# Optimization experiments

Hardware: AMD Instinct MI355X
Metric: run time of the kernel (lower is better)

Reference implementation:

```python
import jax, jax.numpy as jnp
import numpy as np

G, M_PER_GROUP, K, N = 8, 2048, 4096, 4096  # experts, tokens/expert, d_model, expert out dim


def setup_inputs() -> dict:
    key = jax.random.key(0)
    k1, k2, k3, k4 = jax.random.split(key, 4)
    T = G * M_PER_GROUP
    # int8 quantized activations [total_tokens, K] and per-expert weights [G, N, K] ('NT' layout)
    i8_left_tensor = jax.random.randint(k1, (T, K), -127, 128, dtype=jnp.int32).astype(jnp.int8)
    i8_right_tensors = jax.random.randint(k2, (G, N, K), -127, 128, dtype=jnp.int32).astype(jnp.int8)
    # per-token and per-(group, out-channel) dequant scales
    left_scales = jax.random.uniform(k3, (T,), jnp.float32, 0.001, 0.02)
    right_scales = jax.random.uniform(k4, (G, N), jnp.float32, 0.001, 0.02)
    tokens_per_group = jnp.full((G,), M_PER_GROUP, dtype=jnp.int32)
    return {
        "i8_left_tensor": i8_left_tensor,
        "i8_right_tensors": i8_right_tensors,
        "left_scales": left_scales,
        "right_scales": right_scales,
        "tokens_per_group": tokens_per_group,
    }


def reference(i8_left_tensor, i8_right_tensors, left_scales, right_scales, tokens_per_group):
    # moe_w8a8_group_gemm, 'NT': per group g, out_g = (A_g @ B_g^T) * ls_g[:, None] * rs_g[None, :] -> fp16
    g, n, k = i8_right_tensors.shape
    t = i8_left_tensor.shape[0]
    m = t // g  # equal-sized groups (tokens_per_group is constant M_PER_GROUP)
    a = i8_left_tensor.reshape(g, m, k).astype(jnp.float32)   # [G, M, K]
    b = i8_right_tensors.astype(jnp.float32)                  # [G, N, K]
    acc = jnp.einsum('gmk,gnk->gmn', a, b)                    # int8xint8 accum in f32
    ls = left_scales.reshape(g, m, 1)
    rs = right_scales[:, None, :]
    out = (acc * ls * rs).astype(jnp.float16)                 # fused dequant epilogue
    return out.reshape(t, n)
```

## Files before the change

kernel.cpp:

```cpp
#include <hip/hip_runtime.h>

#define GG 8
#define MPG 2048
#define KD 4096
#define ND 4096

using i32x4 = __attribute__((ext_vector_type(4))) int;

__device__ __forceinline__ int pack4(i32x4 v) {
  return (int)((unsigned)(v[0] & 0xff) | ((unsigned)(v[1] & 0xff) << 8) |
               ((unsigned)(v[2] & 0xff) << 16) | ((unsigned)(v[3] & 0xff) << 24));
}

__global__ void conv_kernel(const int* __restrict__ src, char* __restrict__ dst, long nelem) {
  long t = (long)blockIdx.x * blockDim.x + threadIdx.x;
  long stride = (long)gridDim.x * blockDim.x;
  for (long e = t * 16; e < nelem; e += stride * 16) {
    i32x4 x0 = *(const i32x4*)(src + e);
    i32x4 x1 = *(const i32x4*)(src + e + 4);
    i32x4 x2 = *(const i32x4*)(src + e + 8);
    i32x4 x3 = *(const i32x4*)(src + e + 12);
    i32x4 p;
    p[0] = pack4(x0); p[1] = pack4(x1); p[2] = pack4(x2); p[3] = pack4(x3);
    *(i32x4*)(dst + e) = p;
  }
}

__device__ __forceinline__ void gload_lds16(const void* g, void* l) {
  __builtin_amdgcn_global_load_lds(
      (const __attribute__((address_space(1))) unsigned int*)g,
      (__attribute__((address_space(3))) unsigned int*)l, 16, 0, 0);
}

constexpr int NT = KD / 128;

__global__ __launch_bounds__(512, 2) void gemm256_i8(
    const char* __restrict__ Aall,
    const char* __restrict__ Ball,
    const float* __restrict__ ls,
    const float* __restrict__ rs,
    float* __restrict__ out,
    int g0, int nwg)
{
  extern __shared__ char lds[];

  const int tid  = threadIdx.x;
  const int lane = tid & 63;
  const int wave = tid >> 6;

  int bid = blockIdx.x;
  int wg  = (bid & 7) * (nwg >> 3) + (bid >> 3);
  const int gl = wg >> 7;
  const int rr_ = wg & 127;
  const int bm = (rr_ >> 4) * 256;
  const int bn = (rr_ & 15) * 256;
  const int g  = g0 + gl;

  const int srow = tid >> 3;
  const int scol = ((tid & 7) << 4) ^ ((srow & 7) << 4);
  const char* Ag = Aall + ((size_t)gl * MPG + bm) * KD;
  const char* Bg = Ball + ((size_t)gl * ND  + bn) * KD;
  const char* pa[4]; const char* pb[4];
#pragma unroll
  for (int i = 0; i < 4; ++i) {
    pa[i] = Ag + (size_t)(i * 64 + srow) * KD + scol;
    pb[i] = Bg + (size_t)(i * 64 + srow) * KD + scol;
  }
  char* wbase = lds + wave * 1024;

  auto stage = [&](int buf, int kt) {
    const int ko = kt << 7;
    char* d = wbase + buf * 65536;
#pragma unroll
    for (int i = 0; i < 4; ++i) gload_lds16(pa[i] + ko, d + i * 8192);
#pragma unroll
    for (int i = 0; i < 4; ++i) gload_lds16(pb[i] + ko, d + 32768 + i * 8192);
  };

  const int wm = wave >> 2;
  const int wn = wave & 3;
  const int r16 = lane & 15;
  const int klane = (lane >> 4) << 4;
  const int sx = (r16 & 7) << 4;
  const char* aBase0 = lds + (size_t)(wm * 128 + r16) * 128;
  const char* bBase0 = lds + 32768 + (size_t)(wn * 64 + r16) * 128;

  i32x4 acc[8][4] = {};

  auto compute = [&](int buf) {
    const char* pA = aBase0 + buf * 65536;
    const char* pB = bBase0 + buf * 65536;
#pragma unroll
    for (int ks = 0; ks < 2; ++ks) {
      const int kx = ((ks << 6) + klane) ^ sx;
      i32x4 bf[4], af[8];
#pragma unroll
      for (int n = 0; n < 4; ++n) bf[n] = *(const i32x4*)(pB + n * 2048 + kx);
#pragma unroll
      for (int m = 0; m < 8; ++m) af[m] = *(const i32x4*)(pA + m * 2048 + kx);
      __builtin_amdgcn_s_setprio(1);
#pragma unroll
      for (int m = 0; m < 8; ++m)
#pragma unroll
        for (int n = 0; n < 4; ++n)
          acc[m][n] = __builtin_amdgcn_mfma_i32_16x16x64_i8(af[m], bf[n], acc[m][n], 0, 0, 0);
      __builtin_amdgcn_s_setprio(0);
    }
  };

  stage(0, 0);
  stage(1, 1);
#pragma unroll 1
  for (int kt = 0; kt < NT; ++kt) {
    const int cur = kt & 1;
    if (kt + 1 < NT) { asm volatile("s_waitcnt vmcnt(8)" ::: "memory"); }
    else             { asm volatile("s_waitcnt vmcnt(0)" ::: "memory"); }
    __builtin_amdgcn_s_barrier();
    asm volatile("" ::: "memory");
    compute(cur);
    asm volatile("" ::: "memory");
    __builtin_amdgcn_s_barrier();
    asm volatile("" ::: "memory");
    if (kt + 2 < NT) stage(cur, kt + 2);
  }

  const size_t orow0 = (size_t)g * MPG + bm + wm * 128 + ((lane >> 4) << 2);
  const int col0 = bn + wn * 64 + r16;
  float rsv[4];
#pragma unroll
  for (int n = 0; n < 4; ++n) rsv[n] = rs[(size_t)g * ND + col0 + n * 16];
#pragma unroll
  for (int m = 0; m < 8; ++m) {
#pragma unroll
    for (int q = 0; q < 4; ++q) {
      size_t row = orow0 + m * 16 + q;
      float lsv = ls[row];
#pragma unroll
      for (int n = 0; n < 4; ++n)
        out[row * ND + col0 + n * 16] = (float)acc[m][n][q] * lsv * rsv[n];
    }
  }
}

constexpr int BM = 128, BN = 128, BK = 64;

template<bool DIRECT>
__global__ __launch_bounds__(256) void gemm_i8(
    const void* __restrict__ Aptr, const void* __restrict__ Bptr,
    const float* __restrict__ ls, const float* __restrict__ rs,
    float* __restrict__ out, int g0)
{
  __shared__ char lA[BM * BK];
  __shared__ char lB[BN * BK];

  const int gl = blockIdx.z;
  const int g = g0 + gl;
  const int bm = blockIdx.y * BM;
  const int bn = blockIdx.x * BN;
  const int tid = threadIdx.x;
  const int lane = tid & 63;
  const int wave = tid >> 6;
  const int wr = (wave >> 1) * 64;
  const int wc = (wave & 1) * 64;
  const int r16 = lane & 15;
  const int kb = (lane >> 4) * 16;

  i32x4 acc[4][4] = {};

  if constexpr (!DIRECT) {
    const char* Ag = (const char*)Aptr + ((size_t)gl * MPG + bm) * KD;
    const char* Bg = (const char*)Bptr + ((size_t)gl * ND + bn) * KD;
    const int srow = tid >> 2;
    const int skoff = (tid & 3) * 16;
    const char* pa0 = Ag + (size_t)srow * KD + skoff;
    const char* pa1 = Ag + (size_t)(srow + 64) * KD + skoff;
    const char* pb0 = Bg + (size_t)srow * KD + skoff;
    const char* pb1 = Bg + (size_t)(srow + 64) * KD + skoff;
    char* la0 = lA + wave * 1024;
    char* la1 = lA + 4096 + wave * 1024;
    char* lb0 = lB + wave * 1024;
    char* lb1 = lB + 4096 + wave * 1024;

    for (int k0 = 0; k0 < KD; k0 += BK) {
      gload_lds16(pa0 + k0, la0);
      gload_lds16(pa1 + k0, la1);
      gload_lds16(pb0 + k0, lb0);
      gload_lds16(pb1 + k0, lb1);
      __syncthreads();
      i32x4 af[4], bf[4];
#pragma unroll
      for (int m = 0; m < 4; ++m) af[m] = *(const i32x4*)(lA + (wr + m * 16 + r16) * BK + kb);
#pragma unroll
      for (int n = 0; n < 4; ++n) bf[n] = *(const i32x4*)(lB + (wc + n * 16 + r16) * BK + kb);
#pragma unroll
      for (int m = 0; m < 4; ++m)
#pragma unroll
        for (int n = 0; n < 4; ++n)
          acc[m][n] = __builtin_amdgcn_mfma_i32_16x16x64_i8(af[m], bf[n], acc[m][n], 0, 0, 0);
      __syncthreads();
    }
  } else {
    const int* Ag = (const int*)Aptr + ((size_t)gl * MPG + bm) * KD;
    const int* Bg = (const int*)Bptr + ((size_t)gl * ND + bn) * KD;
    const int drow = tid >> 1;
    const int dk = (tid & 1) * 32;

    for (int k0 = 0; k0 < KD; k0 += BK) {
      int pa[8], pb[8];
#pragma unroll
      for (int j = 0; j < 8; ++j) pa[j] = pack4(*(const i32x4*)(Ag + (size_t)drow * KD + k0 + dk + j * 4));
#pragma unroll
      for (int j = 0; j < 8; ++j) pb[j] = pack4(*(const i32x4*)(Bg + (size_t)drow * KD + k0 + dk + j * 4));
      __syncthreads();
      *(i32x4*)(lA + drow * 64 + dk)      = *(i32x4*)(pa);
      *(i32x4*)(lA + drow * 64 + dk + 16) = *(i32x4*)(pa + 4);
      *(i32x4*)(lB + drow * 64 + dk)      = *(i32x4*)(pb);
      *(i32x4*)(lB + drow * 64 + dk + 16) = *(i32x4*)(pb + 4);
      __syncthreads();
      i32x4 af[4], bf[4];
#pragma unroll
      for (int m = 0; m < 4; ++m) af[m] = *(const i32x4*)(lA + (wr + m * 16 + r16) * BK + kb);
#pragma unroll
      for (int n = 0; n < 4; ++n) bf[n] = *(const i32x4*)(lB + (wc + n * 16 + r16) * BK + kb);
#pragma unroll
      for (int m = 0; m < 4; ++m)
#pragma unroll
        for (int n = 0; n < 4; ++n)
          acc[m][n] = __builtin_amdgcn_mfma_i32_16x16x64_i8(af[m], bf[n], acc[m][n], 0, 0, 0);
    }
  }

  const size_t trow0 = (size_t)g * MPG + bm + wr + (lane >> 4) * 4;
  const int col0 = bn + wc + r16;
  float rsv[4];
#pragma unroll
  for (int n = 0; n < 4; ++n) rsv[n] = rs[(size_t)g * ND + col0 + n * 16];
#pragma unroll
  for (int m = 0; m < 4; ++m) {
#pragma unroll
    for (int q = 0; q < 4; ++q) {
      size_t row = trow0 + m * 16 + q;
      float lsv = ls[row];
#pragma unroll
      for (int n = 0; n < 4; ++n)
        out[row * ND + col0 + n * 16] = (float)acc[m][n][q] * lsv * rsv[n];
    }
  }
}

extern "C" void kernel_launch(void* const* d_in, const int* in_sizes, int n_in,
                              void* d_out, int out_size, void* d_ws, size_t ws_size,
                              hipStream_t stream) {
  const int* A32 = (const int*)d_in[0];
  const int* B32 = (const int*)d_in[1];
  const float* ls = (const float*)d_in[2];
  const float* rs = (const float*)d_in[3];
  float* out = (float*)d_out;

  const size_t aE = (size_t)GG * MPG * KD;
  const size_t bE = (size_t)GG * ND * KD;
  const size_t aSlab = (size_t)MPG * KD;
  const size_t bSlab = (size_t)ND * KD;

  const int smem = 131072;
  static_assert(131072 == 2 * (32768 + 32768), "lds layout");
  bool big_lds_ok =
      hipFuncSetAttribute((const void*)gemm256_i8,
                          hipFuncAttributeMaxDynamicSharedMemorySize, smem) == hipSuccess;

  if (d_ws && ws_size >= aE + bE) {
    char* wsA = (char*)d_ws;
    char* wsB = wsA + aE;
    conv_kernel<<<8192, 256, 0, stream>>>(A32, wsA, (long)aE);
    conv_kernel<<<16384, 256, 0, stream>>>(B32, wsB, (long)bE);
    if (big_lds_ok) {
      gemm256_i8<<<1024, 512, smem, stream>>>(wsA, wsB, ls, rs, out, 0, 1024);
    } else {
      dim3 grid(ND / BN, MPG / BM, GG);
      gemm_i8<false><<<grid, dim3(256), 0, stream>>>(wsA, wsB, ls, rs, out, 0);
    }
  } else if (d_ws && ws_size >= aSlab + bSlab) {
    char* wsA = (char*)d_ws;
    char* wsB = wsA + aSlab;
    for (int gidx = 0; gidx < GG; ++gidx) {
      conv_kernel<<<2048, 256, 0, stream>>>(A32 + (size_t)gidx * aSlab, wsA, (long)aSlab);
      conv_kernel<<<4096, 256, 0, stream>>>(B32 + (size_t)gidx * bSlab, wsB, (long)bSlab);
      if (big_lds_ok) {
        gemm256_i8<<<128, 512, smem, stream>>>(wsA, wsB, ls, rs, out, gidx, 128);
      } else {
        dim3 grid(ND / BN, MPG / BM, 1);
        gemm_i8<false><<<grid, dim3(256), 0, stream>>>(wsA, wsB, ls, rs, out, gidx);
      }
    }
  } else {
    dim3 grid(ND / BN, MPG / BM, GG);
    gemm_i8<true><<<grid, dim3(256), 0, stream>>>(A32, B32, ls, rs, out, 0);
  }
}
```

Baseline: 499.5 us.

## Split k-tile into four barrier-separated phases with interleaved next-tile prefetch

Restructures the GEMM main loop from a two-stage-ahead double buffer into a one-stage-ahead schedule where each 128-wide k-tile is processed in four phases of 16 MFMAs. The A and B global-to-LDS loads for the next tile are issued in separate phases between LDS fragment reads and MFMA bursts. The intent is to interleave memory issue with compute and reduce register pressure for fragments. The cost is more barriers per iteration and a shallower prefetch, which may expose global load latency.

```diff
diff --git a/kernel.cpp b/kernel.cpp
--- a/kernel.cpp
+++ b/kernel.cpp
@@ -32,6 +32,8 @@
       (__attribute__((address_space(3))) unsigned int*)l, 16, 0, 0);
 }
 
+#define CFENCE() asm volatile("" ::: "memory")
+
 constexpr int NT = KD / 128;
 
 __global__ __launch_bounds__(512, 2) void gemm256_i8(
@@ -68,13 +70,17 @@
   }
   char* wbase = lds + wave * 1024;
 
-  auto stage = [&](int buf, int kt) {
+  auto stageA = [&](int buf, int kt) {
     const int ko = kt << 7;
     char* d = wbase + buf * 65536;
 #pragma unroll
     for (int i = 0; i < 4; ++i) gload_lds16(pa[i] + ko, d + i * 8192);
-#pragma unroll
-    for (int i = 0; i < 4; ++i) gload_lds16(pb[i] + ko, d + 32768 + i * 8192);
+  };
+  auto stageB = [&](int buf, int kt) {
+    const int ko = kt << 7;
+    char* d = wbase + buf * 65536 + 32768;
+#pragma unroll
+    for (int i = 0; i < 4; ++i) gload_lds16(pb[i] + ko, d + i * 8192);
   };
 
   const int wm = wave >> 2;
@@ -87,41 +93,75 @@
 
   i32x4 acc[8][4] = {};
 
-  auto compute = [&](int buf) {
-    const char* pA = aBase0 + buf * 65536;
-    const char* pB = bBase0 + buf * 65536;
-#pragma unroll
-    for (int ks = 0; ks < 2; ++ks) {
-      const int kx = ((ks << 6) + klane) ^ sx;
-      i32x4 bf[4], af[8];
-#pragma unroll
-      for (int n = 0; n < 4; ++n) bf[n] = *(const i32x4*)(pB + n * 2048 + kx);
-#pragma unroll
-      for (int m = 0; m < 8; ++m) af[m] = *(const i32x4*)(pA + m * 2048 + kx);
-      __builtin_amdgcn_s_setprio(1);
-#pragma unroll
-      for (int m = 0; m < 8; ++m)
-#pragma unroll
-        for (int n = 0; n < 4; ++n)
-          acc[m][n] = __builtin_amdgcn_mfma_i32_16x16x64_i8(af[m], bf[n], acc[m][n], 0, 0, 0);
-      __builtin_amdgcn_s_setprio(0);
-    }
-  };
-
-  stage(0, 0);
-  stage(1, 1);
+  stageA(0, 0); stageB(0, 0);
+  asm volatile("s_waitcnt vmcnt(0)" ::: "memory");
+  __builtin_amdgcn_s_barrier();
+  CFENCE();
+
 #pragma unroll 1
   for (int kt = 0; kt < NT; ++kt) {
-    const int cur = kt & 1;
-    if (kt + 1 < NT) { asm volatile("s_waitcnt vmcnt(8)" ::: "memory"); }
-    else             { asm volatile("s_waitcnt vmcnt(0)" ::: "memory"); }
-    __builtin_amdgcn_s_barrier();
-    asm volatile("" ::: "memory");
-    compute(cur);
-    asm volatile("" ::: "memory");
-    __builtin_amdgcn_s_barrier();
-    asm volatile("" ::: "memory");
-    if (kt + 2 < NT) stage(cur, kt + 2);
+    const int c = kt & 1;
+    const char* pA = aBase0 + c * 65536;
+    const char* pB = bBase0 + c * 65536;
+    const int kx0 = klane ^ sx;
+    const int kx1 = (64 + klane) ^ sx;
+    const bool pre = (kt + 1 < NT);
+    i32x4 af[4], bf[4];
+
+#pragma unroll
+    for (int n = 0; n < 4; ++n) bf[n] = *(const i32x4*)(pB + n * 2048 + kx0);
+#pragma unroll
+    for (int m = 0; m < 4; ++m) af[m] = *(const i32x4*)(pA + m * 2048 + kx0);
+    if (pre) stageA(c ^ 1, kt + 1);
+    CFENCE(); __builtin_amdgcn_s_barrier(); CFENCE();
+    __builtin_amdgcn_s_setprio(1);
+#pragma unroll
+    for (int m = 0; m < 4; ++m)
+#pragma unroll
+      for (int n = 0; n < 4; ++n)
+        acc[m][n] = __builtin_amdgcn_mfma_i32_16x16x64_i8(af[m], bf[n], acc[m][n], 0, 0, 0);
+    __builtin_amdgcn_s_setprio(0);
+    CFENCE(); __builtin_amdgcn_s_barrier(); CFENCE();
+
+#pragma unroll
+    for (int m = 0; m < 4; ++m) af[m] = *(const i32x4*)(pA + (4 + m) * 2048 + kx0);
+    if (pre) stageB(c ^ 1, kt + 1);
+    CFENCE(); __builtin_amdgcn_s_barrier(); CFENCE();
+    __builtin_amdgcn_s_setprio(1);
+#pragma unroll
+    for (int m = 0; m < 4; ++m)
+#pragma unroll
+      for (int n = 0; n < 4; ++n)
+        acc[4 + m][n] = __builtin_amdgcn_mfma_i32_16x16x64_i8(af[m], bf[n], acc[4 + m][n], 0, 0, 0);
+    __builtin_amdgcn_s_setprio(0);
+    CFENCE(); __builtin_amdgcn_s_barrier(); CFENCE();
+
+#pragma unroll
+    for (int n = 0; n < 4; ++n) bf[n] = *(const i32x4*)(pB + n * 2048 + kx1);
+#pragma unroll
+    for (int m = 0; m < 4; ++m) af[m] = *(const i32x4*)(pA + m * 2048 + kx1);
+    CFENCE(); __builtin_amdgcn_s_barrier(); CFENCE();
+    __builtin_amdgcn_s_setprio(1);
+#pragma unroll
+    for (int m = 0; m < 4; ++m)
+#pragma unroll
+      for (int n = 0; n < 4; ++n)
+        acc[m][n] = __builtin_amdgcn_mfma_i32_16x16x64_i8(af[m], bf[n], acc[m][n], 0, 0, 0);
+    __builtin_amdgcn_s_setprio(0);
+    CFENCE(); __builtin_amdgcn_s_barrier(); CFENCE();
+
+#pragma unroll
+    for (int m = 0; m < 4; ++m) af[m] = *(const i32x4*)(pA + (4 + m) * 2048 + kx1);
+    asm volatile("s_waitcnt vmcnt(0)" ::: "memory");
+    CFENCE(); __builtin_amdgcn_s_barrier(); CFENCE();
+    __builtin_amdgcn_s_setprio(1);
+#pragma unroll
+    for (int m = 0; m < 4; ++m)
+#pragma unroll
+      for (int n = 0; n < 4; ++n)
+        acc[4 + m][n] = __builtin_amdgcn_mfma_i32_16x16x64_i8(af[m], bf[n], acc[4 + m][n], 0, 0, 0);
+    __builtin_amdgcn_s_setprio(0);
+    CFENCE(); __builtin_amdgcn_s_barrier(); CFENCE();
   }
 
   const size_t orow0 = (size_t)g * MPG + bm + wm * 128 + ((lane >> 4) << 2);
@@ -263,7 +303,6 @@
   const size_t bSlab = (size_t)ND * KD;
 
   const int smem = 131072;
-  static_assert(131072 == 2 * (32768 + 32768), "lds layout");
   bool big_lds_ok =
       hipFuncSetAttribute((const void*)gemm256_i8,
                           hipFuncAttributeMaxDynamicSharedMemorySize, smem) == hipSuccess;
```

Result: faster. 484.5 us (-3.0%).

## Use 4-wave workgroups with 128x128 per-wave tiles for int8 grouped GEMM

Applied to the files above, without the earlier changes.

Reduces the 256x256 tile GEMM from 8 waves to 4 waves, so each wave now computes a 128x128 output sub-tile (8x8 MFMA accumulators) instead of 128x64. This raises arithmetic intensity per LDS fragment load, since each A and B fragment feeds more MFMAs, and halves the barrier participants. In exchange it uses far more accumulator registers (256 VGPRs for acc), gives lower occupancy (launch_bounds 256,1), and adds an explicit lgkmcnt wait and sched_barrier before the end-of-iteration barrier. The staging loop now issues 8 loads per operand per thread, and the conv kernel stride arithmetic is simplified.

```diff
diff --git a/kernel.cpp b/kernel.cpp
--- a/kernel.cpp
+++ b/kernel.cpp
@@ -14,8 +14,8 @@
 
 __global__ void conv_kernel(const int* __restrict__ src, char* __restrict__ dst, long nelem) {
   long t = (long)blockIdx.x * blockDim.x + threadIdx.x;
-  long stride = (long)gridDim.x * blockDim.x;
-  for (long e = t * 16; e < nelem; e += stride * 16) {
+  long stride = (long)gridDim.x * blockDim.x * 16;
+  for (long e = t * 16; e < nelem; e += stride) {
     i32x4 x0 = *(const i32x4*)(src + e);
     i32x4 x1 = *(const i32x4*)(src + e + 4);
     i32x4 x2 = *(const i32x4*)(src + e + 8);
@@ -32,9 +32,11 @@
       (__attribute__((address_space(3))) unsigned int*)l, 16, 0, 0);
 }
 
+#define CFENCE() asm volatile("" ::: "memory")
+
 constexpr int NT = KD / 128;
 
-__global__ __launch_bounds__(512, 2) void gemm256_i8(
+__global__ __launch_bounds__(256, 1) void gemm4w_i8(
     const char* __restrict__ Aall,
     const char* __restrict__ Ball,
     const float* __restrict__ ls,
@@ -60,75 +62,82 @@
   const int scol = ((tid & 7) << 4) ^ ((srow & 7) << 4);
   const char* Ag = Aall + ((size_t)gl * MPG + bm) * KD;
   const char* Bg = Ball + ((size_t)gl * ND  + bn) * KD;
-  const char* pa[4]; const char* pb[4];
-#pragma unroll
-  for (int i = 0; i < 4; ++i) {
-    pa[i] = Ag + (size_t)(i * 64 + srow) * KD + scol;
-    pb[i] = Bg + (size_t)(i * 64 + srow) * KD + scol;
-  }
+  const int voff = srow * KD + scol;
   char* wbase = lds + wave * 1024;
 
   auto stage = [&](int buf, int kt) {
     const int ko = kt << 7;
     char* d = wbase + buf * 65536;
 #pragma unroll
-    for (int i = 0; i < 4; ++i) gload_lds16(pa[i] + ko, d + i * 8192);
-#pragma unroll
-    for (int i = 0; i < 4; ++i) gload_lds16(pb[i] + ko, d + 32768 + i * 8192);
+    for (int i = 0; i < 8; ++i)
+      gload_lds16(Ag + (size_t)(ko + voff) + (size_t)i * (32 * KD), d + i * 4096);
+#pragma unroll
+    for (int i = 0; i < 8; ++i)
+      gload_lds16(Bg + (size_t)(ko + voff) + (size_t)i * (32 * KD), d + 32768 + i * 4096);
   };
 
-  const int wm = wave >> 2;
-  const int wn = wave & 3;
+  const int wm = wave >> 1;
+  const int wn = wave & 1;
   const int r16 = lane & 15;
   const int klane = (lane >> 4) << 4;
   const int sx = (r16 & 7) << 4;
-  const char* aBase0 = lds + (size_t)(wm * 128 + r16) * 128;
-  const char* bBase0 = lds + 32768 + (size_t)(wn * 64 + r16) * 128;
-
-  i32x4 acc[8][4] = {};
-
-  auto compute = [&](int buf) {
-    const char* pA = aBase0 + buf * 65536;
-    const char* pB = bBase0 + buf * 65536;
-#pragma unroll
-    for (int ks = 0; ks < 2; ++ks) {
-      const int kx = ((ks << 6) + klane) ^ sx;
-      i32x4 bf[4], af[8];
-#pragma unroll
-      for (int n = 0; n < 4; ++n) bf[n] = *(const i32x4*)(pB + n * 2048 + kx);
-#pragma unroll
-      for (int m = 0; m < 8; ++m) af[m] = *(const i32x4*)(pA + m * 2048 + kx);
-      __builtin_amdgcn_s_setprio(1);
-#pragma unroll
-      for (int m = 0; m < 8; ++m)
-#pragma unroll
-        for (int n = 0; n < 4; ++n)
-          acc[m][n] = __builtin_amdgcn_mfma_i32_16x16x64_i8(af[m], bf[n], acc[m][n], 0, 0, 0);
-      __builtin_amdgcn_s_setprio(0);
-    }
-  };
+  const int aoff = (wm * 128 + r16) * 128;
+  const int boff = 32768 + (wn * 128 + r16) * 128;
+  const int kx0 = klane ^ sx;
+  const int kx1 = (64 + klane) ^ sx;
+
+  i32x4 acc[8][8] = {};
 
   stage(0, 0);
   stage(1, 1);
+
 #pragma unroll 1
   for (int kt = 0; kt < NT; ++kt) {
-    const int cur = kt & 1;
-    if (kt + 1 < NT) { asm volatile("s_waitcnt vmcnt(8)" ::: "memory"); }
+    const int c = kt & 1;
+    const char* pA = lds + c * 65536 + aoff;
+    const char* pB = lds + c * 65536 + boff;
+
+    if (kt + 1 < NT) { asm volatile("s_waitcnt vmcnt(16)" ::: "memory"); }
     else             { asm volatile("s_waitcnt vmcnt(0)" ::: "memory"); }
     __builtin_amdgcn_s_barrier();
-    asm volatile("" ::: "memory");
-    compute(cur);
-    asm volatile("" ::: "memory");
+    CFENCE();
+
+    i32x4 af[8], bf[8];
+#pragma unroll
+    for (int n = 0; n < 8; ++n) bf[n] = *(const i32x4*)(pB + n * 2048 + kx0);
+#pragma unroll
+    for (int m = 0; m < 8; ++m) af[m] = *(const i32x4*)(pA + m * 2048 + kx0);
+    __builtin_amdgcn_s_setprio(1);
+#pragma unroll
+    for (int m = 0; m < 8; ++m)
+#pragma unroll
+      for (int n = 0; n < 8; ++n)
+        acc[m][n] = __builtin_amdgcn_mfma_i32_16x16x64_i8(af[m], bf[n], acc[m][n], 0, 0, 0);
+    __builtin_amdgcn_s_setprio(0);
+#pragma unroll
+    for (int n = 0; n < 8; ++n) bf[n] = *(const i32x4*)(pB + n * 2048 + kx1);
+#pragma unroll
+    for (int m = 0; m < 8; ++m) af[m] = *(const i32x4*)(pA + m * 2048 + kx1);
+    __builtin_amdgcn_s_setprio(1);
+#pragma unroll
+    for (int m = 0; m < 8; ++m)
+#pragma unroll
+      for (int n = 0; n < 8; ++n)
+        acc[m][n] = __builtin_amdgcn_mfma_i32_16x16x64_i8(af[m], bf[n], acc[m][n], 0, 0, 0);
+    __builtin_amdgcn_s_setprio(0);
+
+    asm volatile("s_waitcnt lgkmcnt(0)" ::: "memory");
+    __builtin_amdgcn_sched_barrier(0);
     __builtin_amdgcn_s_barrier();
-    asm volatile("" ::: "memory");
-    if (kt + 2 < NT) stage(cur, kt + 2);
+    CFENCE();
+    if (kt + 2 < NT) stage(c, kt + 2);
   }
 
   const size_t orow0 = (size_t)g * MPG + bm + wm * 128 + ((lane >> 4) << 2);
-  const int col0 = bn + wn * 64 + r16;
-  float rsv[4];
-#pragma unroll
-  for (int n = 0; n < 4; ++n) rsv[n] = rs[(size_t)g * ND + col0 + n * 16];
+  const int col0 = bn + wn * 128 + r16;
+  float rsv[8];
+#pragma unroll
+  for (int n = 0; n < 8; ++n) rsv[n] = rs[(size_t)g * ND + col0 + n * 16];
 #pragma unroll
   for (int m = 0; m < 8; ++m) {
 #pragma unroll
@@ -136,7 +145,7 @@
       size_t row = orow0 + m * 16 + q;
       float lsv = ls[row];
 #pragma unroll
-      for (int n = 0; n < 4; ++n)
+      for (int n = 0; n < 8; ++n)
         out[row * ND + col0 + n * 16] = (float)acc[m][n][q] * lsv * rsv[n];
     }
   }
@@ -263,9 +272,8 @@
   const size_t bSlab = (size_t)ND * KD;
 
   const int smem = 131072;
-  static_assert(131072 == 2 * (32768 + 32768), "lds layout");
   bool big_lds_ok =
-      hipFuncSetAttribute((const void*)gemm256_i8,
+      hipFuncSetAttribute((const void*)gemm4w_i8,
                           hipFuncAttributeMaxDynamicSharedMemorySize, smem) == hipSuccess;
 
   if (d_ws && ws_size >= aE + bE) {
@@ -274,7 +282,7 @@
     conv_kernel<<<8192, 256, 0, stream>>>(A32, wsA, (long)aE);
     conv_kernel<<<16384, 256, 0, stream>>>(B32, wsB, (long)bE);
     if (big_lds_ok) {
-      gemm256_i8<<<1024, 512, smem, stream>>>(wsA, wsB, ls, rs, out, 0, 1024);
+      gemm4w_i8<<<1024, 256, smem, stream>>>(wsA, wsB, ls, rs, out, 0, 1024);
     } else {
       dim3 grid(ND / BN, MPG / BM, GG);
       gemm_i8<false><<<grid, dim3(256), 0, stream>>>(wsA, wsB, ls, rs, out, 0);
@@ -286,7 +294,7 @@
       conv_kernel<<<2048, 256, 0, stream>>>(A32 + (size_t)gidx * aSlab, wsA, (long)aSlab);
       conv_kernel<<<4096, 256, 0, stream>>>(B32 + (size_t)gidx * bSlab, wsB, (long)bSlab);
       if (big_lds_ok) {
-        gemm256_i8<<<128, 512, smem, stream>>>(wsA, wsB, ls, rs, out, gidx, 128);
+        gemm4w_i8<<<128, 256, smem, stream>>>(wsA, wsB, ls, rs, out, gidx, 128);
       } else {
         dim3 grid(ND / BN, MPG / BM, 1);
         gemm_i8<false><<<grid, dim3(256), 0, stream>>>(wsA, wsB, ls, rs, out, gidx);
```

Result: slower. 618.1 us (+23.7%).
